# Kernel optimization log

Hardware: AMD Instinct MI355X
Metric: run time of the kernel (lower is better)

The kernel has to match this reference:

```python
import jax, jax.numpy as jnp
import numpy as np

N_CLASS = 20
N_SIGMA = 2
H = W = 512
B = 4
N_INST = 32
W_INST, W_VAR, W_SEED = 1.0, 10.0, 1.0
FG_WEIGHT = 10.0


def _xym():
    # channel 0: x along width, channel 1: y along height (matches torch buffer)
    xm = jnp.broadcast_to(jnp.linspace(0.0, 1.0, W)[None, :], (H, W))
    ym = jnp.broadcast_to(jnp.linspace(0.0, 1.0, H)[:, None], (H, W))
    return jnp.stack([xm, ym], axis=0)  # [2, H, W]


def lovasz_hinge_flat(logits, gt, valid):
    # logits, gt (0/1 float), valid (bool), all flat [P]; ignored pixels excluded
    P = logits.shape[0]
    vf = valid.astype(logits.dtype)
    signs = 2.0 * gt - 1.0
    # push ignored pixels to the end of the descending sort; relu(-1e9)=0 kills them
    errors = jnp.where(valid, 1.0 - logits * signs, -1e9)
    errors_sorted, perm = jax.lax.top_k(errors, P)  # descending
    gt_sorted = jnp.take(gt * vf, perm)
    v_sorted = jnp.take(vf, perm)
    gts = jnp.sum(gt * vf)
    inter = gts - jnp.cumsum(gt_sorted)
    union = gts + jnp.cumsum((1.0 - gt_sorted) * v_sorted)
    jac = 1.0 - inter / jnp.maximum(union, 1e-9)
    jac = jnp.concatenate([jac[:1], jac[1:] - jac[:-1]])
    return jnp.sum(jax.nn.relu(errors_sorted) * jac)


def _per_image(pred_b, inst_b, lab_b, xym, fg_w, n_inst):
    spatial_emb = jnp.tanh(pred_b[:2]) + xym            # [2,H,W]
    sigma = pred_b[2:2 + N_SIGMA]                       # [n_sigma,H,W]
    seed = jax.nn.sigmoid(pred_b[2 + N_SIGMA:2 + N_SIGMA + N_CLASS])  # [C,H,W]
    inst = inst_b[0]
    lab = lab_b[0]
    valid = (lab != 255)

    # background seed loss: sum over classes of seed^2 on pixels not of that class
    cls_ids = jnp.arange(N_CLASS)
    bg = (lab[None] != (cls_ids + 1)[:, None, None]) & valid[None]
    seed_bg = jnp.sum(jnp.square(seed) * bg)

    def per_inst(iid):
        m = (inst == iid)
        mf = m.astype(pred_b.dtype)
        cnt = jnp.maximum(jnp.sum(mf), 1.0)
        # to_center=True: center is mean coordinate of instance pixels
        center = jnp.sum(xym * mf[None], axis=(1, 2)) / cnt          # [2]
        s_mean = jnp.sum(sigma * mf[None], axis=(1, 2)) / cnt        # [n_sigma]
        var_l = jnp.sum(jnp.square(sigma - jax.lax.stop_gradient(s_mean)[:, None, None]) * mf[None]) / (N_SIGMA * cnt)
        s = jnp.exp(s_mean * 10.0)
        dist = jnp.exp(-jnp.sum(jnp.square(spatial_emb - center[:, None, None]) * s[:, None, None], axis=0))  # [H,W]
        inst_l = lovasz_hinge_flat((dist * 2.0 - 1.0).reshape(-1), mf.reshape(-1), valid.reshape(-1))
        cls = jnp.max(lab * m) - 1  # instance class (0-indexed)
        seed_c = jnp.take(seed, cls, axis=0)
        seed_fg = jnp.take(fg_w, cls) * jnp.sum(jnp.square(seed_c - jax.lax.stop_gradient(dist)) * mf)
        return inst_l, var_l, seed_fg

    inst_ls, var_ls, seed_fgs = jax.vmap(per_inst)(jnp.arange(1, n_inst + 1))
    instance_loss = jnp.sum(inst_ls) / n_inst
    var_loss = jnp.sum(var_ls) / n_inst
    seed_loss = (seed_bg + jnp.sum(seed_fgs)) / (H * W)
    return W_INST * instance_loss + W_VAR * var_loss + W_SEED * seed_loss


def setup_inputs() -> dict:
    key = jax.random.key(0)
    k1, k2 = jax.random.split(key)
    prediction = jax.random.normal(k1, (B, 2 + N_SIGMA + N_CLASS, H, W), dtype=jnp.float32)
    instances = jax.random.randint(k2, (B, 1, H, W), 0, N_INST + 1).astype(jnp.int32)
    # each instance id has a consistent class, as the torch instance_to_cls dict assumes
    labels = jnp.where(instances > 0, ((instances - 1) % N_CLASS) + 1, 0).astype(jnp.int32)
    return {"prediction": prediction, "instances": instances, "labels": labels, "n_instances": N_INST}


def reference(prediction, instances, labels, n_instances):
    xym = _xym()
    fg_w = jnp.full((N_CLASS,), FG_WEIGHT, dtype=prediction.dtype)
    per = jax.vmap(lambda p, i, l: _per_image(p, i, l, xym, fg_w, n_instances))(prediction, instances, labels)
    return jnp.mean(per) + jnp.sum(prediction) * 0.0
```

## Files before the change

### kernel.cpp

```cpp
#include <hip/hip_runtime.h>
#include <hip/hip_fp16.h>
#include <math.h>

#define HH 512
#define WW 512
#define BB 4
#define NCLS 20
#define NINST 32
#define NPIX (HH*WW)
#define NCH 24
#define NBIN 64
#define NCHUNK3 128
#define CPX3 2048
#define K3T 512
#define HSTR 33

#define OFF_PARTA  ((size_t)0)
#define OFF_PSEED  (OFF_PARTA + 1024*256*4)
#define OFF_PARTV  (OFF_PSEED + 10240*4)
#define OFF_STATS  (OFF_PARTV + 1024*4)
#define OFF_SEEDBG (OFF_STATS + 8*128*4)
#define OFF_VALID  (OFF_SEEDBG + 4*4)
#define OFF_SFG    (OFF_VALID + 4*4)
#define OFF_RECXY  ((OFF_SFG + 512*4 + 255) & ~(size_t)255)
#define OFF_META   (OFF_RECXY + (size_t)BB*NPIX*4)
#define OFF_SGOWN  (OFF_META + (size_t)BB*NPIX)
#define OFF_LAB8   (OFF_SGOWN + (size_t)BB*NPIX)
#define OFF_HIST   (OFF_LAB8 + (size_t)BB*NPIX)

__device__ __forceinline__ float fast_rcp(float x) { return __builtin_amdgcn_rcpf(x); }
__device__ __forceinline__ float fast_sigmoid(float z) { return fast_rcp(1.0f + __expf(-z)); }
__device__ __forceinline__ float fast_tanh(float x) {
  return 1.0f - 2.0f * fast_rcp(__expf(2.0f * x) + 1.0f);
}

__global__ __launch_bounds__(256) void k0_geom(
    const float* __restrict__ pred, const int* __restrict__ inst,
    const int* __restrict__ lab,
    float* __restrict__ partA, float* __restrict__ partV,
    unsigned* __restrict__ recxy, unsigned char* __restrict__ meta8,
    unsigned char* __restrict__ lab8, float* __restrict__ outz)
{
  __shared__ unsigned s_st[4][NINST][9];
  __shared__ float s_valid;
  int t = threadIdx.x;
  int w = t >> 6;
  for (int i = t; i < 4*NINST*9; i += 256) ((unsigned*)s_st)[i] = 0u;
  if (t == 0) s_valid = 0.f;
  if (blockIdx.x == 0 && t == 0) outz[0] = 0.f;
  __syncthreads();

  int b = blockIdx.x >> 8;
  int p = (blockIdx.x & 255) * 1024 + t * 4;
  const float* pb = pred + (size_t)b*NCH*NPIX;
  float4 e0v = *(const float4*)(pb + p);
  float4 e1v = *(const float4*)(pb + NPIX + p);
  float4 g0v = *(const float4*)(pb + 2*NPIX + p);
  float4 g1v = *(const float4*)(pb + 3*NPIX + p);
  int4 idv = *(const int4*)(inst + (size_t)b*NPIX + p);
  int4 lbv = *(const int4*)(lab + (size_t)b*NPIX + p);

  float vloc = 0.f;
  #pragma unroll
  for (int u = 0; u < 4; ++u) {
    int px = p + u;
    int x = px & (WW-1);
    int y = px >> 9;
    float xm = x * (1.0f/(WW-1));
    float ym = y * (1.0f/(HH-1));
    float g0 = (&g0v.x)[u];
    float g1 = (&g1v.x)[u];
    int id = (&idv.x)[u];
    int lb = (&lbv.x)[u];
    if (lb != 255) vloc += 1.0f;
    if (id >= 1) {
      int j = id - 1;
      unsigned* row = s_st[w][j];
      atomicAdd(&row[0], 1u | ((lb != 255) ? 0x10000u : 0u));
      atomicAdd((float*)&row[1], xm);
      atomicAdd((float*)&row[2], ym);
      atomicAdd((float*)&row[3], g0);
      atomicAdd((float*)&row[4], g1);
      atomicAdd((float*)&row[5], g0*g0);
      atomicAdd((float*)&row[6], g1*g1);
    }
  }

  {
    unsigned rx[4], mpk = 0, lpk = 0;
    #pragma unroll
    for (int u = 0; u < 4; ++u) {
      int px = p + u;
      int x = px & (WW-1);
      int y = px >> 9;
      float ex = fast_tanh((&e0v.x)[u]) + x * (1.0f/(WW-1));
      float ey = fast_tanh((&e1v.x)[u]) + y * (1.0f/(HH-1));
      __half2 h = __floats2half2_rn(ex, ey);
      rx[u] = *reinterpret_cast<unsigned*>(&h);
      int lb = (&lbv.x)[u];
      unsigned valid = (lb != 255) ? 1u : 0u;
      mpk |= ((unsigned)((&idv.x)[u]) | (valid << 7)) << (8*u);
      lpk |= ((unsigned)(unsigned char)lb) << (8*u);
    }
    *(uint4*)(recxy + (size_t)b*NPIX + p) = make_uint4(rx[0], rx[1], rx[2], rx[3]);
    *(unsigned*)(meta8 + (size_t)b*NPIX + p) = mpk;
    *(unsigned*)(lab8 + (size_t)b*NPIX + p) = lpk;
  }
  for (int o = 32; o; o >>= 1) vloc += __shfl_down(vloc, o);
  if ((t & 63) == 0) atomicAdd(&s_valid, vloc);
  __syncthreads();

  {
    int j = t & 31, f = t >> 5;
    float v;
    if (f == 0) {
      unsigned s = (s_st[0][j][0] & 0xFFFFu) + (s_st[1][j][0] & 0xFFFFu)
                 + (s_st[2][j][0] & 0xFFFFu) + (s_st[3][j][0] & 0xFFFFu);
      v = (float)s;
    } else if (f == 7) {
      unsigned s = (s_st[0][j][0] >> 16) + (s_st[1][j][0] >> 16)
                 + (s_st[2][j][0] >> 16) + (s_st[3][j][0] >> 16);
      v = (float)s;
    } else {
      v = __uint_as_float(s_st[0][j][f]) + __uint_as_float(s_st[1][j][f])
        + __uint_as_float(s_st[2][j][f]) + __uint_as_float(s_st[3][j][f]);
    }
    partA[(blockIdx.x << 8) + t] = v;
  }
  if (t == 0) partV[blockIdx.x] = s_valid;
}

__global__ __launch_bounds__(256) void k1_seed(
    const float* __restrict__ pred, const unsigned char* __restrict__ lab8,
    float* __restrict__ partSeed, unsigned char* __restrict__ sgown)
{
  __shared__ float s_seed;
  int t = threadIdx.x;
  if (t == 0) s_seed = 0.f;
  __syncthreads();
  int b = blockIdx.y;
  int c = blockIdx.x >> 7;
  int chunk = blockIdx.x & 127;
  int base = chunk*2048 + t*8;
  const float* ch = pred + ((size_t)b*NCH + 4 + c)*NPIX;
  float4 v0 = *(const float4*)(ch + base);
  float4 v1 = *(const float4*)(ch + base + 4);
  uint2 lb2 = *(const uint2*)(lab8 + (size_t)b*NPIX + base);
  unsigned cp1 = (unsigned)(c + 1);

  float local = 0.f;
  #pragma unroll
  for (int k = 0; k < 8; ++k) {
    float z = (k < 4) ? (&v0.x)[k] : (&v1.x)[k-4];
    unsigned lb = ((k < 4 ? lb2.x : lb2.y) >> (8*(k & 3))) & 0xFFu;
    float sg = fast_sigmoid(z);
    bool own = (lb == cp1);
    if (lb != 255u && !own) local += sg*sg;
    if (own) sgown[(size_t)b*NPIX + base + k] = (unsigned char)(sg*255.f + 0.5f);
  }
  for (int o = 32; o; o >>= 1) local += __shfl_down(local, o);
  if ((t & 63) == 0) atomicAdd(&s_seed, local);
  __syncthreads();
  if (t == 0) partSeed[(b*20 + c)*128 + chunk] = s_seed;
}

__global__ __launch_bounds__(256) void k2a_reduce(
    const float* __restrict__ partA, const float* __restrict__ partSeed,
    const float* __restrict__ partV,
    float* __restrict__ stats, float* __restrict__ seedbg,
    float* __restrict__ validT)
{
  int bid = blockIdx.x;
  int t = threadIdx.x;
  if (bid < 32) {
    __shared__ float red[256];
    int b = bid >> 3, f = bid & 7;
    int j = t & 31, grp = t >> 5;
    float s = 0.f;
    #pragma unroll 8
    for (int k = 0; k < 32; ++k)
      s += partA[((b*256 + grp*32 + k) << 8) + (f << 5) + j];
    red[t] = s; __syncthreads();
    for (int st = 128; st >= 32; st >>= 1) {
      if (t < st) red[t] += red[t + st];
      __syncthreads();
    }
    if (t < 32) stats[f*128 + b*32 + t] = red[t];
  } else {
    int img = t >> 6, lane = t & 63;
    float s = 0.f, v = 0.f;
    #pragma unroll 8
    for (int k = 0; k < 40; ++k)
      s += partSeed[img*2560 + lane*40 + k];
    #pragma unroll
    for (int k = 0; k < 4; ++k)
      v += partV[img*256 + lane*4 + k];
    for (int o = 32; o; o >>= 1) {
      s += __shfl_down(s, o);
      v += __shfl_down(v, o);
    }
    if (lane == 0) { seedbg[img] = s; validT[img] = v; }
  }
}

__global__ __launch_bounds__(K3T) void k3_hist(
    const unsigned* __restrict__ recxy, const unsigned char* __restrict__ meta8,
    const unsigned char* __restrict__ sgown, const float* __restrict__ stats,
    unsigned* __restrict__ hist, float* __restrict__ sfg)
{
  __shared__ unsigned hc[NBIN*HSTR];
  __shared__ float sder[NINST][4];
  __shared__ float s_fg[8];
  int t = threadIdx.x;
  int bid = blockIdx.x;
  int b = bid >> 7;
  int chunk = bid & 127;
  for (int i = t; i < NBIN*HSTR; i += K3T) hc[i] = 0u;
  if (t < NINST) {
    int pr = b*NINST + t;
    float cnt = fmaxf(stats[0*128+pr], 1.0f);
    float rc = fast_rcp(cnt);
    sder[t][0] = stats[1*128+pr] * rc;
    sder[t][1] = stats[2*128+pr] * rc;
    sder[t][2] = -1.442695041f * __expf(10.f * stats[3*128+pr] * rc);
    sder[t][3] = -1.442695041f * __expf(10.f * stats[4*128+pr] * rc);
  }
  __syncthreads();

  int w = t >> 6, lane = t & 63;
  int j = lane & 31, jp1 = j + 1;
  float cx = sder[j][0], cy = sder[j][1];
  float s0 = sder[j][2], s1 = sder[j][3];
  size_t cbase = (size_t)b*NPIX + chunk*CPX3;
  int off = w*256 + ((lane >> 5) << 1);
  unsigned* hrow = hc + j;
  float fg = 0.f;

  #pragma unroll 4
  for (int r = 0; r < 64; ++r) {
    int p0 = off + r*4;
    uint2 xy = *(const uint2*)(recxy + cbase + p0);
    unsigned short mm = *(const unsigned short*)(meta8 + cbase + p0);
    unsigned short ss = *(const unsigned short*)(sgown + cbase + p0);
    #pragma unroll
    for (int u = 0; u < 2; ++u) {
      unsigned lo = u ? xy.y : xy.x;
      unsigned meta = (mm >> (8*u)) & 0xFFu;
      __half2 h;
      *reinterpret_cast<unsigned*>(&h) = lo;
      float2 e = __half22float2(h);
      float dx = e.x - cx, dy = e.y - cy;
      float dist = exp2f(dx*dx*s0 + dy*dy*s1);
      bool own = ((int)(meta & 0x3Fu) == jp1);
      if (own) {
        float sg = (float)((ss >> (8*u)) & 0xFFu) * (1.0f/255.f);
        float d = sg - dist; fg += d*d;
      }
      if (meta & 0x80u) {
        float f = own ? (1.0f - dist) : dist;
        unsigned bin = min((unsigned)(f * (float)NBIN), NBIN-1u);
        if (bin) atomicAdd(&hrow[bin*HSTR], own ? 0x10001u : 1u);
      }
    }
  }
  for (int o = 32; o; o >>= 1) fg += __shfl_down(fg, o);
  if (lane == 0) s_fg[w] = fg;
  __syncthreads();
  if (t == 0) {
    float s = 0.f;
    #pragma unroll
    for (int i = 0; i < 8; ++i) s += s_fg[i];
    sfg[bid] = 10.0f * s;
  }
  unsigned* out = hist + (size_t)(b*NCHUNK3 + chunk) * (NINST*NBIN);
  #pragma unroll
  for (int k = 0; k < NINST*NBIN/K3T; ++k) {
    int idx = k*K3T + t;
    out[idx] = hc[(idx & 63)*HSTR + (idx >> 6)];
  }
}

__global__ __launch_bounds__(512) void k4_final(
    const unsigned* __restrict__ hist, const float* __restrict__ stats,
    const float* __restrict__ validT, const float* __restrict__ seedbg,
    const float* __restrict__ sfg, float* __restrict__ out)
{
  __shared__ unsigned s_c[8][NBIN], s_p[8][NBIN];
  __shared__ unsigned rc[NBIN], rp[NBIN];
  __shared__ float s_L;
  int t = threadIdx.x;
  int pair = blockIdx.x;
  int b = pair >> 5, j = pair & 31;
  int grp = t >> 6, bin = t & 63;
  const unsigned* bp = hist + ((size_t)b*NCHUNK3*NINST + j)*NBIN + bin;
  unsigned c = 0, p = 0;
  #pragma unroll 8
  for (int ch = grp*16; ch < grp*16 + 16; ++ch) {
    unsigned v = bp[(size_t)ch * (NINST*NBIN)];
    c += v & 0xFFFFu; p += v >> 16;
  }
  s_c[grp][bin] = c; s_p[grp][bin] = p;
  __syncthreads();
  if (t < NBIN) {
    unsigned cc = 0, pp = 0;
    #pragma unroll
    for (int g = 0; g < 8; ++g) { cc += s_c[g][t]; pp += s_p[g][t]; }
    s_c[0][t] = cc; s_p[0][t] = pp;
    rc[t] = t ? cc : 0u; rp[t] = t ? pp : 0u;
  }
  __syncthreads();
  for (int st = 32; st; st >>= 1) {
    if (t < st) { rc[t] += rc[t+st]; rp[t] += rp[t+st]; }
    __syncthreads();
  }
  float G = stats[7*128+pair];
  if (t == 0) {
    s_c[0][0] = (unsigned)validT[b] - rc[0];
    s_p[0][0] = (unsigned)G - rp[0];
  }
  __syncthreads();

  if (t < 64) {
    int lane = t;
    int k = NBIN - 1 - lane;
    unsigned n = s_c[0][k], pp0 = s_p[0][k];
    for (int off = 1; off < 64; off <<= 1) {
      unsigned nn = __shfl_up(n, off);
      unsigned pq = __shfl_up(pp0, off);
      if (lane >= off) { n += nn; pp0 += pq; }
    }
    float fN = (float)n;
    float fP = (float)pp0;
    float uni = G + fN - fP;
    float J = 1.0f - (G - fP) / fmaxf(uni, 1e-9f);
    float Jp = __shfl_up(J, 1);
    if (lane == 0) Jp = 0.f;
    float v = (k + 0.5f) * (2.0f/NBIN);
    float L = v * (J - Jp);
    for (int o = 32; o; o >>= 1) L += __shfl_down(L, o);
    if (lane == 0) s_L = L;
  }
  __syncthreads();
  if (t == 0) {
    float cntA = stats[0*128+pair];
    float cnt = fmaxf(cntA, 1.0f);
    float s0 = stats[3*128+pair], s1 = stats[4*128+pair];
    float q0 = stats[5*128+pair], q1 = stats[6*128+pair];
    float sm0 = s0/cnt, sm1 = s1/cnt;
    float varnum = q0 - 2.f*sm0*s0 + cntA*sm0*sm0
                 + q1 - 2.f*sm1*s1 + cntA*sm1*sm1;
    float varl = varnum / (2.0f * cnt);
    atomicAdd(out, (s_L + 10.0f*varl) * (1.0f/(NINST*BB)));
  }
  if (pair == 0) {
    __shared__ float red[512];
    float acc = sfg[t];
    if (t < 4) acc += seedbg[t];
    red[t] = acc; __syncthreads();
    for (int st = 256; st; st >>= 1) {
      if (t < st) red[t] += red[t+st];
      __syncthreads();
    }
    if (t == 0) atomicAdd(out, red[0] * (1.0f/((float)NPIX*BB)));
  }
}

extern "C" void kernel_launch(void* const* d_in, const int* in_sizes, int n_in,
                              void* d_out, int out_size, void* d_ws, size_t ws_size,
                              hipStream_t stream)
{
  const float* pred = (const float*)d_in[0];
  const int* inst = (const int*)d_in[1];
  const int* lab  = (const int*)d_in[2];
  char* ws = (char*)d_ws;
  float* partA = (float*)(ws + OFF_PARTA);
  float* partSeed = (float*)(ws + OFF_PSEED);
  float* partV = (float*)(ws + OFF_PARTV);
  float* stats = (float*)(ws + OFF_STATS);
  float* seedbg = (float*)(ws + OFF_SEEDBG);
  float* validT = (float*)(ws + OFF_VALID);
  float* sfg = (float*)(ws + OFF_SFG);
  unsigned* recxy = (unsigned*)(ws + OFF_RECXY);
  unsigned char* meta8 = (unsigned char*)(ws + OFF_META);
  unsigned char* sgown = (unsigned char*)(ws + OFF_SGOWN);
  unsigned char* lab8 = (unsigned char*)(ws + OFF_LAB8);
  unsigned* hist = (unsigned*)(ws + OFF_HIST);

  hipLaunchKernelGGL(k0_geom, dim3(1024), dim3(256), 0, stream,
                     pred, inst, lab, partA, partV, recxy, meta8, lab8,
                     (float*)d_out);
  hipLaunchKernelGGL(k1_seed, dim3(20*128, BB), dim3(256), 0, stream,
                     pred, lab8, partSeed, sgown);
  hipLaunchKernelGGL(k2a_reduce, dim3(33), dim3(256), 0, stream,
                     partA, partSeed, partV, stats, seedbg, validT);
  hipLaunchKernelGGL(k3_hist, dim3(BB*NCHUNK3), dim3(K3T), 0, stream,
                     recxy, meta8, sgown, stats, hist, sfg);
  hipLaunchKernelGGL(k4_final, dim3(128), dim3(512), 0, stream,
                     hist, stats, validT, seedbg, sfg, (float*)d_out);
}
```

Before: 98.22 us.

## Fuse seed sigmoid pass into histogram kernel and pack per-pixel records

Removes the separate seed kernel. The histogram kernel now reads the 20 class channels for its chunk, computes the background seed sum and the own-class sigmoid itself, and keeps the quantised values in shared memory instead of a global sgown buffer. The geometry kernel writes one packed 8-byte record per pixel (half2 embedding plus label/id/valid) in place of three separate arrays. This removes a kernel launch and the global round trips for lab8 and sgown. In exchange, the histogram kernel carries the 20-channel read and sigmoid work with fewer blocks (512) than the old seed kernel had, which may lower memory-level parallelism for that phase.

After: 98.99 us. Within noise of the previous version (+0.8%).

```diff
diff --git a/kernel.cpp b/kernel.cpp
--- a/kernel.cpp
+++ b/kernel.cpp
@@ -16,17 +16,12 @@
 #define HSTR 33
 
 #define OFF_PARTA  ((size_t)0)
-#define OFF_PSEED  (OFF_PARTA + 1024*256*4)
-#define OFF_PARTV  (OFF_PSEED + 10240*4)
+#define OFF_PARTV  (OFF_PARTA + 1024*256*4)
 #define OFF_STATS  (OFF_PARTV + 1024*4)
-#define OFF_SEEDBG (OFF_STATS + 8*128*4)
-#define OFF_VALID  (OFF_SEEDBG + 4*4)
-#define OFF_SFG    (OFF_VALID + 4*4)
-#define OFF_RECXY  ((OFF_SFG + 512*4 + 255) & ~(size_t)255)
-#define OFF_META   (OFF_RECXY + (size_t)BB*NPIX*4)
-#define OFF_SGOWN  (OFF_META + (size_t)BB*NPIX)
-#define OFF_LAB8   (OFF_SGOWN + (size_t)BB*NPIX)
-#define OFF_HIST   (OFF_LAB8 + (size_t)BB*NPIX)
+#define OFF_VALID  (OFF_STATS + 8*128*4)
+#define OFF_SFG2   (OFF_VALID + 4*4)
+#define OFF_REC    ((OFF_SFG2 + 512*8 + 255) & ~(size_t)255)
+#define OFF_HIST   (OFF_REC + (size_t)BB*NPIX*8)
 
 __device__ __forceinline__ float fast_rcp(float x) { return __builtin_amdgcn_rcpf(x); }
 __device__ __forceinline__ float fast_sigmoid(float z) { return fast_rcp(1.0f + __expf(-z)); }
@@ -34,12 +29,11 @@
   return 1.0f - 2.0f * fast_rcp(__expf(2.0f * x) + 1.0f);
 }
 
-__global__ __launch_bounds__(256) void k0_geom(
+__global__ __launch_bounds__(256) void k1_geom(
     const float* __restrict__ pred, const int* __restrict__ inst,
     const int* __restrict__ lab,
     float* __restrict__ partA, float* __restrict__ partV,
-    unsigned* __restrict__ recxy, unsigned char* __restrict__ meta8,
-    unsigned char* __restrict__ lab8, float* __restrict__ outz)
+    uint2* __restrict__ rec, float* __restrict__ outz)
 {
   __shared__ unsigned s_st[4][NINST][9];
   __shared__ float s_valid;
@@ -87,7 +81,7 @@
   }
 
   {
-    unsigned rx[4], mpk = 0, lpk = 0;
+    uint2 r4[4];
     #pragma unroll
     for (int u = 0; u < 4; ++u) {
       int px = p + u;
@@ -96,15 +90,15 @@
       float ex = fast_tanh((&e0v.x)[u]) + x * (1.0f/(WW-1));
       float ey = fast_tanh((&e1v.x)[u]) + y * (1.0f/(HH-1));
       __half2 h = __floats2half2_rn(ex, ey);
-      rx[u] = *reinterpret_cast<unsigned*>(&h);
       int lb = (&lbv.x)[u];
       unsigned valid = (lb != 255) ? 1u : 0u;
-      mpk |= ((unsigned)((&idv.x)[u]) | (valid << 7)) << (8*u);
-      lpk |= ((unsigned)(unsigned char)lb) << (8*u);
-    }
-    *(uint4*)(recxy + (size_t)b*NPIX + p) = make_uint4(rx[0], rx[1], rx[2], rx[3]);
-    *(unsigned*)(meta8 + (size_t)b*NPIX + p) = mpk;
-    *(unsigned*)(lab8 + (size_t)b*NPIX + p) = lpk;
+      unsigned meta = (unsigned)(&idv.x)[u] | (valid << 7);
+      r4[u].x = *reinterpret_cast<unsigned*>(&h);
+      r4[u].y = (unsigned)(unsigned char)lb | (meta << 8);
+    }
+    uint4* dst = (uint4*)(rec + (size_t)b*NPIX + p);
+    dst[0] = make_uint4(r4[0].x, r4[0].y, r4[1].x, r4[1].y);
+    dst[1] = make_uint4(r4[2].x, r4[2].y, r4[3].x, r4[3].y);
   }
   for (int o = 32; o; o >>= 1) vloc += __shfl_down(vloc, o);
   if ((t & 63) == 0) atomicAdd(&s_valid, vloc);
@@ -130,45 +124,9 @@
   if (t == 0) partV[blockIdx.x] = s_valid;
 }
 
-__global__ __launch_bounds__(256) void k1_seed(
-    const float* __restrict__ pred, const unsigned char* __restrict__ lab8,
-    float* __restrict__ partSeed, unsigned char* __restrict__ sgown)
-{
-  __shared__ float s_seed;
-  int t = threadIdx.x;
-  if (t == 0) s_seed = 0.f;
-  __syncthreads();
-  int b = blockIdx.y;
-  int c = blockIdx.x >> 7;
-  int chunk = blockIdx.x & 127;
-  int base = chunk*2048 + t*8;
-  const float* ch = pred + ((size_t)b*NCH + 4 + c)*NPIX;
-  float4 v0 = *(const float4*)(ch + base);
-  float4 v1 = *(const float4*)(ch + base + 4);
-  uint2 lb2 = *(const uint2*)(lab8 + (size_t)b*NPIX + base);
-  unsigned cp1 = (unsigned)(c + 1);
-
-  float local = 0.f;
-  #pragma unroll
-  for (int k = 0; k < 8; ++k) {
-    float z = (k < 4) ? (&v0.x)[k] : (&v1.x)[k-4];
-    unsigned lb = ((k < 4 ? lb2.x : lb2.y) >> (8*(k & 3))) & 0xFFu;
-    float sg = fast_sigmoid(z);
-    bool own = (lb == cp1);
-    if (lb != 255u && !own) local += sg*sg;
-    if (own) sgown[(size_t)b*NPIX + base + k] = (unsigned char)(sg*255.f + 0.5f);
-  }
-  for (int o = 32; o; o >>= 1) local += __shfl_down(local, o);
-  if ((t & 63) == 0) atomicAdd(&s_seed, local);
-  __syncthreads();
-  if (t == 0) partSeed[(b*20 + c)*128 + chunk] = s_seed;
-}
-
 __global__ __launch_bounds__(256) void k2a_reduce(
-    const float* __restrict__ partA, const float* __restrict__ partSeed,
-    const float* __restrict__ partV,
-    float* __restrict__ stats, float* __restrict__ seedbg,
-    float* __restrict__ validT)
+    const float* __restrict__ partA, const float* __restrict__ partV,
+    float* __restrict__ stats, float* __restrict__ validT)
 {
   int bid = blockIdx.x;
   int t = threadIdx.x;
@@ -188,29 +146,24 @@
     if (t < 32) stats[f*128 + b*32 + t] = red[t];
   } else {
     int img = t >> 6, lane = t & 63;
-    float s = 0.f, v = 0.f;
-    #pragma unroll 8
-    for (int k = 0; k < 40; ++k)
-      s += partSeed[img*2560 + lane*40 + k];
+    float v = 0.f;
     #pragma unroll
     for (int k = 0; k < 4; ++k)
       v += partV[img*256 + lane*4 + k];
-    for (int o = 32; o; o >>= 1) {
-      s += __shfl_down(s, o);
-      v += __shfl_down(v, o);
-    }
-    if (lane == 0) { seedbg[img] = s; validT[img] = v; }
+    for (int o = 32; o; o >>= 1) v += __shfl_down(v, o);
+    if (lane == 0) validT[img] = v;
   }
 }
 
 __global__ __launch_bounds__(K3T) void k3_hist(
-    const unsigned* __restrict__ recxy, const unsigned char* __restrict__ meta8,
-    const unsigned char* __restrict__ sgown, const float* __restrict__ stats,
-    unsigned* __restrict__ hist, float* __restrict__ sfg)
+    const float* __restrict__ pred, const uint2* __restrict__ rec,
+    const float* __restrict__ stats,
+    unsigned* __restrict__ hist, float2* __restrict__ sfg2)
 {
   __shared__ unsigned hc[NBIN*HSTR];
+  __shared__ unsigned char sgbuf[CPX3];
   __shared__ float sder[NINST][4];
-  __shared__ float s_fg[8];
+  __shared__ float s_fg[8], s_sd[8];
   int t = threadIdx.x;
   int bid = blockIdx.x;
   int b = bid >> 7;
@@ -225,38 +178,64 @@
     sder[t][2] = -1.442695041f * __expf(10.f * stats[3*128+pr] * rc);
     sder[t][3] = -1.442695041f * __expf(10.f * stats[4*128+pr] * rc);
   }
-  __syncthreads();
-
+
+  size_t cbase = (size_t)b*NPIX + chunk*CPX3;
+  int p1 = t*4;
+  uint4 rr0 = *(const uint4*)(rec + cbase + p1);
+  uint4 rr1 = *(const uint4*)(rec + cbase + p1 + 2);
+  unsigned ry[4] = {rr0.y, rr0.w, rr1.y, rr1.w};
+  const float* pbs = pred + (size_t)b*NCH*NPIX + chunk*CPX3 + p1;
+  float sg4[4] = {0.f,0.f,0.f,0.f};
+  float seedloc = 0.f;
+  for (int c = 0; c < NCLS; ++c) {
+    float4 sv = *(const float4*)(pbs + (size_t)(4+c)*NPIX);
+    #pragma unroll
+    for (int u = 0; u < 4; ++u) {
+      float sg = fast_sigmoid((&sv.x)[u]);
+      unsigned lb = ry[u] & 0xFFu;
+      if (lb == (unsigned)(c+1)) sg4[u] = sg;
+      else if (ry[u] & 0x8000u) seedloc += sg*sg;
+    }
+  }
+  {
+    unsigned pk = 0;
+    #pragma unroll
+    for (int u = 0; u < 4; ++u)
+      pk |= ((unsigned)(unsigned char)(sg4[u]*255.f + 0.5f)) << (8*u);
+    ((unsigned*)sgbuf)[t] = pk;
+  }
   int w = t >> 6, lane = t & 63;
+  for (int o = 32; o; o >>= 1) seedloc += __shfl_down(seedloc, o);
+  if (lane == 0) s_sd[w] = seedloc;
+  __syncthreads();
+
   int j = lane & 31, jp1 = j + 1;
   float cx = sder[j][0], cy = sder[j][1];
   float s0 = sder[j][2], s1 = sder[j][3];
-  size_t cbase = (size_t)b*NPIX + chunk*CPX3;
-  int off = w*256 + ((lane >> 5) << 1);
+  const uint4* base4 = (const uint4*)(rec + cbase) + w*128 + (lane >> 5);
+  int pxoff = w*256 + ((lane >> 5) << 1);
   unsigned* hrow = hc + j;
   float fg = 0.f;
 
   #pragma unroll 4
   for (int r = 0; r < 64; ++r) {
-    int p0 = off + r*4;
-    uint2 xy = *(const uint2*)(recxy + cbase + p0);
-    unsigned short mm = *(const unsigned short*)(meta8 + cbase + p0);
-    unsigned short ss = *(const unsigned short*)(sgown + cbase + p0);
+    uint4 rv = base4[r*2];
+    unsigned short spk = *(const unsigned short*)(sgbuf + pxoff + r*4);
     #pragma unroll
     for (int u = 0; u < 2; ++u) {
-      unsigned lo = u ? xy.y : xy.x;
-      unsigned meta = (mm >> (8*u)) & 0xFFu;
+      unsigned lo = u ? rv.z : rv.x;
+      unsigned hi = u ? rv.w : rv.y;
       __half2 h;
       *reinterpret_cast<unsigned*>(&h) = lo;
       float2 e = __half22float2(h);
       float dx = e.x - cx, dy = e.y - cy;
       float dist = exp2f(dx*dx*s0 + dy*dy*s1);
-      bool own = ((int)(meta & 0x3Fu) == jp1);
+      bool own = ((int)((hi >> 8) & 0x3Fu) == jp1);
       if (own) {
-        float sg = (float)((ss >> (8*u)) & 0xFFu) * (1.0f/255.f);
+        float sg = (float)((spk >> (8*u)) & 0xFFu) * (1.0f/255.f);
         float d = sg - dist; fg += d*d;
       }
-      if (meta & 0x80u) {
+      if (hi & 0x8000u) {
         float f = own ? (1.0f - dist) : dist;
         unsigned bin = min((unsigned)(f * (float)NBIN), NBIN-1u);
         if (bin) atomicAdd(&hrow[bin*HSTR], own ? 0x10001u : 1u);
@@ -267,10 +246,10 @@
   if (lane == 0) s_fg[w] = fg;
   __syncthreads();
   if (t == 0) {
-    float s = 0.f;
-    #pragma unroll
-    for (int i = 0; i < 8; ++i) s += s_fg[i];
-    sfg[bid] = 10.0f * s;
+    float f = 0.f, s = 0.f;
+    #pragma unroll
+    for (int i = 0; i < 8; ++i) { f += s_fg[i]; s += s_sd[i]; }
+    sfg2[bid] = make_float2(10.0f * f, s);
   }
   unsigned* out = hist + (size_t)(b*NCHUNK3 + chunk) * (NINST*NBIN);
   #pragma unroll
@@ -282,8 +261,8 @@
 
 __global__ __launch_bounds__(512) void k4_final(
     const unsigned* __restrict__ hist, const float* __restrict__ stats,
-    const float* __restrict__ validT, const float* __restrict__ seedbg,
-    const float* __restrict__ sfg, float* __restrict__ out)
+    const float* __restrict__ validT, const float2* __restrict__ sfg2,
+    float* __restrict__ out)
 {
   __shared__ unsigned s_c[8][NBIN], s_p[8][NBIN];
   __shared__ unsigned rc[NBIN], rp[NBIN];
@@ -354,9 +333,9 @@
   }
   if (pair == 0) {
     __shared__ float red[512];
-    float acc = sfg[t];
-    if (t < 4) acc += seedbg[t];
-    red[t] = acc; __syncthreads();
+    float2 sf = sfg2[t];
+    red[t] = sf.x + sf.y;
+    __syncthreads();
     for (int st = 256; st; st >>= 1) {
       if (t < st) red[t] += red[t+st];
       __syncthreads();
@@ -374,27 +353,19 @@
   const int* lab  = (const int*)d_in[2];
   char* ws = (char*)d_ws;
   float* partA = (float*)(ws + OFF_PARTA);
-  float* partSeed = (float*)(ws + OFF_PSEED);
   float* partV = (float*)(ws + OFF_PARTV);
   float* stats = (float*)(ws + OFF_STATS);
-  float* seedbg = (float*)(ws + OFF_SEEDBG);
   float* validT = (float*)(ws + OFF_VALID);
-  float* sfg = (float*)(ws + OFF_SFG);
-  unsigned* recxy = (unsigned*)(ws + OFF_RECXY);
-  unsigned char* meta8 = (unsigned char*)(ws + OFF_META);
-  unsigned char* sgown = (unsigned char*)(ws + OFF_SGOWN);
-  unsigned char* lab8 = (unsigned char*)(ws + OFF_LAB8);
+  float2* sfg2 = (float2*)(ws + OFF_SFG2);
+  uint2* rec = (uint2*)(ws + OFF_REC);
   unsigned* hist = (unsigned*)(ws + OFF_HIST);
 
-  hipLaunchKernelGGL(k0_geom, dim3(1024), dim3(256), 0, stream,
-                     pred, inst, lab, partA, partV, recxy, meta8, lab8,
-                     (float*)d_out);
-  hipLaunchKernelGGL(k1_seed, dim3(20*128, BB), dim3(256), 0, stream,
-                     pred, lab8, partSeed, sgown);
+  hipLaunchKernelGGL(k1_geom, dim3(1024), dim3(256), 0, stream,
+                     pred, inst, lab, partA, partV, rec, (float*)d_out);
   hipLaunchKernelGGL(k2a_reduce, dim3(33), dim3(256), 0, stream,
-                     partA, partSeed, partV, stats, seedbg, validT);
+                     partA, partV, stats, validT);
   hipLaunchKernelGGL(k3_hist, dim3(BB*NCHUNK3), dim3(K3T), 0, stream,
-                     recxy, meta8, sgown, stats, hist, sfg);
+                     pred, rec, stats, hist, sfg2);
   hipLaunchKernelGGL(k4_final, dim3(128), dim3(512), 0, stream,
-                     hist, stats, validT, seedbg, sfg, (float*)d_out);
-}
+                     hist, stats, validT, sfg2, (float*)d_out);
+}
```
